# Kernel optimization log

Hardware: AMD Instinct MI355X
Metric: run time of the kernel (lower is better)

The kernel has to match this reference:

```python
import jax, jax.numpy as jnp
import numpy as np

N_NODES = 50000
N_EDGES = 800000
N_FEAT = 128
HIDDEN = 128
N_GRAPHS = 256


def gcn_conv(x, W, b, src, dst, n_nodes):
    # PyG GCNConv, add_self_loops=False, edge_weight=1:
    # out_i = sum_{(j->i)} d_j^{-1/2} d_i^{-1/2} (x_j @ W) + b, deg over target idx
    h = x @ W                                    # [N, out]
    deg = jax.ops.segment_sum(jnp.ones((src.shape[0],), h.dtype), dst,
                              num_segments=n_nodes)          # [N]
    dis = jnp.where(deg > 0, jax.lax.rsqrt(jnp.maximum(deg, 1.0)), 0.0)
    norm = dis[src] * dis[dst]                   # [E]
    msg = h[src] * norm[:, None]                 # [E, out] gather + scale
    out = jax.ops.segment_sum(msg, dst, num_segments=n_nodes)  # scatter-add
    return out + b


def setup_inputs() -> dict:
    key = jax.random.key(0)
    ks = jax.random.split(key, 12)
    x = jax.random.normal(ks[0], (N_NODES, N_FEAT), jnp.float32)
    edge_index = jax.random.randint(ks[1], (2, N_EDGES), 0, N_NODES, jnp.int64)
    batch = jnp.sort(jax.random.randint(ks[2], (N_NODES,), 0, N_GRAPHS, jnp.int64))

    def glorot(k, shape):
        lim = float(np.sqrt(6.0 / (shape[0] + shape[1])))
        return jax.random.uniform(k, shape, jnp.float32, -lim, lim)

    W1 = glorot(ks[3], (N_FEAT, HIDDEN)); b1 = jnp.zeros((HIDDEN,), jnp.float32)
    W2 = glorot(ks[4], (HIDDEN, HIDDEN)); b2 = jnp.zeros((HIDDEN,), jnp.float32)
    Wf1 = glorot(ks[5], (HIDDEN, HIDDEN // 2)); bf1 = jnp.zeros((HIDDEN // 2,), jnp.float32)
    Wl = glorot(ks[6], (HIDDEN // 2, 2)); bl = jnp.zeros((2,), jnp.float32)
    return {"x": x, "edge_index": edge_index, "batch": batch,
            "W1": W1, "b1": b1, "W2": W2, "b2": b2,
            "Wf1": Wf1, "bf1": bf1, "Wl": Wl, "bl": bl}


def reference(x, edge_index, batch, W1, b1, W2, b2, Wf1, bf1, Wl, bl):
    src, dst = edge_index[0], edge_index[1]
    h = jax.nn.relu(gcn_conv(x, W1, b1, src, dst, N_NODES))
    h = jax.nn.relu(gcn_conv(h, W2, b2, src, dst, N_NODES))
    h = gcn_conv(h, W2, b2, src, dst, N_NODES)   # conv2 applied a second time (same weights)
    # global_mean_pool over graphs
    sums = jax.ops.segment_sum(h, batch, num_segments=N_GRAPHS)      # [G, H]
    cnts = jax.ops.segment_sum(jnp.ones((h.shape[0],), h.dtype), batch,
                               num_segments=N_GRAPHS)                # [G]
    g = sums / jnp.maximum(cnts, 1.0)[:, None]
    g = jax.nn.relu(g @ Wf1 + bf1)
    logits = g @ Wl + bl
    return jax.nn.softmax(logits, axis=1)
```

## Files before the change

### kernel.cpp

```cpp
#include <hip/hip_runtime.h>
#include <hip/hip_bf16.h>

#define N_NODES 50000
#define N_EDGES 800000
#define NF 128
#define NG 256
#define CAP 64

typedef unsigned short ushort_t;
typedef __attribute__((ext_vector_type(8))) short bf16x8;
typedef __attribute__((ext_vector_type(4))) float f32x4;

__device__ __forceinline__ float b2f(ushort_t u) {
    union { unsigned i; float f; } x; x.i = ((unsigned)u) << 16; return x.f;
}
__device__ __forceinline__ ushort_t f2b(float f) {
    union { float f; unsigned i; } x; x.f = f;
    unsigned r = (x.i + 0x7fffu + ((x.i >> 16) & 1u)) >> 16;
    return (ushort_t)r;
}

__global__ void k_fill_pad(const int* __restrict__ src, const int* __restrict__ dst,
                           int* __restrict__ cur, ushort_t* __restrict__ csr_pad, int E) {
    int e = blockIdx.x * blockDim.x + threadIdx.x;
    if (e < E) {
        int d = dst[e];
        int p = atomicAdd(&cur[d], 1);
        if (p < CAP) csr_pad[d * CAP + p] = (ushort_t)src[e];
    }
}

__global__ void k_dis(const int* __restrict__ cur, float* __restrict__ dis, int n) {
    int i = blockIdx.x * blockDim.x + threadIdx.x;
    if (i < n) {
        int c = cur[i];
        dis[i] = (c > 0) ? rsqrtf((float)c) : 0.f;
    }
}

__global__ void k_cvt_x(const float* __restrict__ in, ushort_t* __restrict__ out, int n4) {
    int i = blockIdx.x * blockDim.x + threadIdx.x;
    if (i < n4) {
        float4 v = *(const float4*)&in[i * 4];
        ushort4 o;
        o.x = f2b(v.x); o.y = f2b(v.y); o.z = f2b(v.z); o.w = f2b(v.w);
        *(ushort4*)&out[i * 4] = o;
    }
}

__global__ void k_prep_w(const float* __restrict__ W, ushort_t* __restrict__ Wt_hi,
                         ushort_t* __restrict__ Wt_lo) {
    int t = blockIdx.x * blockDim.x + threadIdx.x;
    int k = t >> 7, c = t & 127;
    float w = W[k * 128 + c];
    ushort_t hi = f2b(w);
    ushort_t lo = f2b(w - b2f(hi));
    Wt_hi[c * 128 + k] = hi;
    Wt_lo[c * 128 + k] = lo;
}

__global__ __launch_bounds__(256) void k_gemm_mfma(
        const ushort_t* __restrict__ Xb, const ushort_t* __restrict__ Wt_hi,
        const ushort_t* __restrict__ Wt_lo, const float* __restrict__ dis,
        ushort_t* __restrict__ Yb, int n) {
    __shared__ ushort_t Wlds[2][16384];
    int t = threadIdx.x;
    {
        const int4* gh = (const int4*)Wt_hi;
        const int4* gl = (const int4*)Wt_lo;
        int4* sh = (int4*)&Wlds[0][0];
        int4* sl = (int4*)&Wlds[1][0];
#pragma unroll
        for (int i = 0; i < 8; ++i) {
            int u = t + i * 256;
            int swz = u ^ ((u >> 4) & 7);
            sh[swz] = gh[u];
            sl[swz] = gl[u];
        }
    }
    __syncthreads();

    int wid = t >> 6;
    int l   = t & 63;
    int la  = l & 15;
    int kb  = l >> 4;
    int r0  = blockIdx.x * 64 + wid * 16;

    bf16x8 a[4];
    {
        int ra = min(r0 + la, n - 1);
        const ushort_t* xrow = Xb + (size_t)ra * 128 + kb * 8;
#pragma unroll
        for (int kt = 0; kt < 4; ++kt)
            a[kt] = *(const bf16x8*)(xrow + kt * 32);
    }

    f32x4 acc[8];
#pragma unroll
    for (int ct = 0; ct < 8; ++ct) acc[ct] = (f32x4){0.f, 0.f, 0.f, 0.f};

#pragma unroll
    for (int ct = 0; ct < 8; ++ct) {
        int c = ct * 16 + la;
        int ubase = c * 128 + kb * 8;
        int sw = (c & 7) << 3;
#pragma unroll
        for (int kt = 0; kt < 4; ++kt) {
            int u16 = (ubase + kt * 32) ^ sw;
            bf16x8 bh = *(const bf16x8*)&Wlds[0][u16];
            bf16x8 bl = *(const bf16x8*)&Wlds[1][u16];
            acc[ct] = __builtin_amdgcn_mfma_f32_16x16x32_bf16(a[kt], bh, acc[ct], 0, 0, 0);
            acc[ct] = __builtin_amdgcn_mfma_f32_16x16x32_bf16(a[kt], bl, acc[ct], 0, 0, 0);
        }
    }

    float dsc[4];
#pragma unroll
    for (int j = 0; j < 4; ++j)
        dsc[j] = dis[min(r0 + kb * 4 + j, n - 1)];

    __syncthreads();
    ushort_t* tile = ((ushort_t*)Wlds) + wid * 2048;
#pragma unroll
    for (int ct = 0; ct < 8; ++ct) {
        int cc = ct * 16 + la;
#pragma unroll
        for (int j = 0; j < 4; ++j)
            tile[(kb * 4 + j) * 128 + cc] = f2b(acc[ct][j] * dsc[j]);
    }
    __syncthreads();
    {
        const int4* t4 = (const int4*)tile;
        int4* dst4 = (int4*)(Yb + (size_t)r0 * 128);
#pragma unroll
        for (int i = 0; i < 4; ++i) {
            int u = l * 4 + i;
            int row = u >> 4;
            if (r0 + row < n) dst4[u] = t4[u];
        }
    }
}

template <bool RELU>
__global__ __launch_bounds__(256) void k_agg(
        const ushort_t* __restrict__ Hs, const int* __restrict__ cur,
        const ushort_t* __restrict__ csr_pad, const float* __restrict__ dis,
        const float* __restrict__ bias, ushort_t* __restrict__ out, int n) {
    int lane = threadIdx.x & 31;
    int sub  = threadIdx.x >> 5;
    int node = blockIdx.x * 8 + sub;
    if (node >= n) return;
    int deg = min(cur[node], CAP);
    const ushort_t* lst = csr_pad + (size_t)node * CAP;
    int c0 = lane * 4;

    float4 a0 = make_float4(0.f, 0.f, 0.f, 0.f);
    float4 a1 = make_float4(0.f, 0.f, 0.f, 0.f);
    float4 a2 = make_float4(0.f, 0.f, 0.f, 0.f);
    float4 a3 = make_float4(0.f, 0.f, 0.f, 0.f);
    int p = 0;
    for (; p + 3 < deg; p += 4) {
        int j0 = lst[p], j1 = lst[p + 1], j2 = lst[p + 2], j3 = lst[p + 3];
        ushort4 v0 = *(const ushort4*)&Hs[(size_t)j0 * 128 + c0];
        ushort4 v1 = *(const ushort4*)&Hs[(size_t)j1 * 128 + c0];
        ushort4 v2 = *(const ushort4*)&Hs[(size_t)j2 * 128 + c0];
        ushort4 v3 = *(const ushort4*)&Hs[(size_t)j3 * 128 + c0];
        a0.x += b2f(v0.x); a0.y += b2f(v0.y); a0.z += b2f(v0.z); a0.w += b2f(v0.w);
        a1.x += b2f(v1.x); a1.y += b2f(v1.y); a1.z += b2f(v1.z); a1.w += b2f(v1.w);
        a2.x += b2f(v2.x); a2.y += b2f(v2.y); a2.z += b2f(v2.z); a2.w += b2f(v2.w);
        a3.x += b2f(v3.x); a3.y += b2f(v3.y); a3.z += b2f(v3.z); a3.w += b2f(v3.w);
    }
    for (; p < deg; ++p) {
        int j = lst[p];
        ushort4 v = *(const ushort4*)&Hs[(size_t)j * 128 + c0];
        a0.x += b2f(v.x); a0.y += b2f(v.y); a0.z += b2f(v.z); a0.w += b2f(v.w);
    }
    float dsc = dis[node];
    float4 b = *(const float4*)&bias[c0];
    float rx = ((a0.x + a1.x) + (a2.x + a3.x)) * dsc + b.x;
    float ry = ((a0.y + a1.y) + (a2.y + a3.y)) * dsc + b.y;
    float rz = ((a0.z + a1.z) + (a2.z + a3.z)) * dsc + b.z;
    float rw = ((a0.w + a1.w) + (a2.w + a3.w)) * dsc + b.w;
    if (RELU) {
        rx = fmaxf(rx, 0.f); ry = fmaxf(ry, 0.f);
        rz = fmaxf(rz, 0.f); rw = fmaxf(rw, 0.f);
    }
    ushort4 o;
    o.x = f2b(rx); o.y = f2b(ry); o.z = f2b(rz); o.w = f2b(rw);
    *(ushort4*)&out[(size_t)node * 128 + c0] = o;
}

#define POOL_CHUNK 128
__global__ __launch_bounds__(128) void k_pool_partial(
        const ushort_t* __restrict__ H, const int* __restrict__ batch,
        float* __restrict__ gsum, int n) {
    int f = threadIdx.x;
    int s = blockIdx.x * POOL_CHUNK;
    int e = min(s + POOL_CHUNK, n);
    if (s >= n) return;
    float acc = 0.f;
    int g = batch[s];
    for (int i = s; i < e; ++i) {
        int bg = batch[i];
        if (bg != g) {
            atomicAdd(&gsum[g * 128 + f], acc);
            acc = 0.f;
            g = bg;
        }
        acc += b2f(H[(size_t)i * 128 + f]);
    }
    atomicAdd(&gsum[g * 128 + f], acc);
}

__global__ void k_head(const float* __restrict__ gsum, const int* __restrict__ batch,
                       const float* __restrict__ Wf1, const float* __restrict__ bf1,
                       const float* __restrict__ Wl, const float* __restrict__ bl,
                       float* __restrict__ out, int n) {
    int g = blockIdx.x;
    int j = threadIdx.x;
    __shared__ float xs[128];
    __shared__ float hs[64];

    int lo = 0, hi = n;
    while (lo < hi) { int m = (lo + hi) >> 1; if (batch[m] < g) lo = m + 1; else hi = m; }
    int s0 = lo;
    hi = n;
    while (lo < hi) { int m = (lo + hi) >> 1; if (batch[m] <= g) lo = m + 1; else hi = m; }
    float inv_cnt = 1.f / fmaxf((float)(lo - s0), 1.f);

    xs[j]      = gsum[g * 128 + j] * inv_cnt;
    xs[j + 64] = gsum[g * 128 + 64 + j] * inv_cnt;
    __syncthreads();
    float acc = bf1[j];
#pragma unroll 4
    for (int k = 0; k < 128; k++) acc += xs[k] * Wf1[k * 64 + j];
    hs[j] = fmaxf(acc, 0.f);
    __syncthreads();
    if (j == 0) {
        float l0 = bl[0], l1 = bl[1];
        for (int k = 0; k < 64; k++) { l0 += hs[k] * Wl[k * 2 + 0]; l1 += hs[k] * Wl[k * 2 + 1]; }
        float m  = fmaxf(l0, l1);
        float e0 = expf(l0 - m), e1 = expf(l1 - m);
        float inv = 1.f / (e0 + e1);
        out[g * 2 + 0] = e0 * inv;
        out[g * 2 + 1] = e1 * inv;
    }
}

extern "C" void kernel_launch(void* const* d_in, const int* in_sizes, int n_in,
                              void* d_out, int out_size, void* d_ws, size_t ws_size,
                              hipStream_t stream) {
    const float* x    = (const float*)d_in[0];
    const int*   eidx = (const int*)d_in[1];
    const int*   batch= (const int*)d_in[2];
    const float* W1   = (const float*)d_in[3];
    const float* b1   = (const float*)d_in[4];
    const float* W2   = (const float*)d_in[5];
    const float* b2   = (const float*)d_in[6];
    const float* Wf1  = (const float*)d_in[7];
    const float* bf1  = (const float*)d_in[8];
    const float* Wl   = (const float*)d_in[9];
    const float* bl   = (const float*)d_in[10];
    float* out = (float*)d_out;

    const int* src = eidx;
    const int* dst = eidx + N_EDGES;

    char* w = (char*)d_ws;
    auto alloc = [&](size_t bytes) -> void* {
        void* p = (void*)w;
        w += (bytes + 255) & ~(size_t)255;
        return p;
    };
    ushort_t* xb     = (ushort_t*)alloc((size_t)N_NODES * NF * 2);
    ushort_t* Yb     = (ushort_t*)alloc((size_t)N_NODES * NF * 2);
    ushort_t* Hb     = (ushort_t*)alloc((size_t)N_NODES * NF * 2);
    ushort_t* W1h    = (ushort_t*)alloc((size_t)NF * NF * 2);
    ushort_t* W1l    = (ushort_t*)alloc((size_t)NF * NF * 2);
    ushort_t* W2h    = (ushort_t*)alloc((size_t)NF * NF * 2);
    ushort_t* W2l    = (ushort_t*)alloc((size_t)NF * NF * 2);
    float*    dis    = (float*)alloc((size_t)N_NODES * 4);
    int*      cur    = (int*)  alloc((size_t)N_NODES * 4);
    ushort_t* csr_pad= (ushort_t*)alloc((size_t)N_NODES * CAP * 2);
    float*    gsum   = (float*)alloc((size_t)NG * NF * 4);

    hipMemsetAsync(cur, 0, (size_t)N_NODES * 4, stream);
    hipMemsetAsync(gsum, 0, (size_t)NG * NF * 4, stream);

    k_fill_pad<<<(N_EDGES + 255) / 256, 256, 0, stream>>>(src, dst, cur, csr_pad, N_EDGES);
    k_dis<<<(N_NODES + 255) / 256, 256, 0, stream>>>(cur, dis, N_NODES);

    k_cvt_x<<<(N_NODES * NF / 4 + 255) / 256, 256, 0, stream>>>(x, xb, N_NODES * NF / 4);
    k_prep_w<<<64, 256, 0, stream>>>(W1, W1h, W1l);
    k_prep_w<<<64, 256, 0, stream>>>(W2, W2h, W2l);

    int gb = (N_NODES + 63) / 64;
    int ab = (N_NODES + 7) / 8;
    k_gemm_mfma<<<gb, 256, 0, stream>>>(xb, W1h, W1l, dis, Yb, N_NODES);
    k_agg<true><<<ab, 256, 0, stream>>>(Yb, cur, csr_pad, dis, b1, Hb, N_NODES);
    k_gemm_mfma<<<gb, 256, 0, stream>>>(Hb, W2h, W2l, dis, Yb, N_NODES);
    k_agg<true><<<ab, 256, 0, stream>>>(Yb, cur, csr_pad, dis, b2, Hb, N_NODES);
    k_gemm_mfma<<<gb, 256, 0, stream>>>(Hb, W2h, W2l, dis, Yb, N_NODES);
    k_agg<false><<<ab, 256, 0, stream>>>(Yb, cur, csr_pad, dis, b2, Hb, N_NODES);

    k_pool_partial<<<(N_NODES + POOL_CHUNK - 1) / POOL_CHUNK, 128, 0, stream>>>(Hb, batch, gsum, N_NODES);
    k_head<<<NG, 64, 0, stream>>>(gsum, batch, Wf1, bf1, Wl, bl, out, N_NODES);
}
```

Baseline: 262.6 us.

## Build padded CSR with per-block LDS counters and fuse fp32-to-bf16 into first GEMM

Replaces the global-atomic CSR fill, the degree normalization kernel and the memset with one kernel of 64 blocks. Each block owns a node range, scans all destination indices and uses shared-memory atomics to place sources, then writes the clamped degree and rsqrt normalization. It also removes the separate x conversion kernel by loading fp32 x directly in the first GEMM and converting to bf16 in registers. The trade-off is that every build block rereads the full edge list (64x reads of dst), with low parallelism, in exchange for fewer launches and no global atomics.

```diff
diff --git a/kernel.cpp b/kernel.cpp
--- a/kernel.cpp
+++ b/kernel.cpp
@@ -6,6 +6,8 @@
 #define NF 128
 #define NG 256
 #define CAP 64
+#define NB_BUILD 64
+#define NR_PER ((N_NODES + NB_BUILD - 1) / NB_BUILD)
 
 typedef unsigned short ushort_t;
 typedef __attribute__((ext_vector_type(8))) short bf16x8;
@@ -20,31 +22,38 @@
     return (ushort_t)r;
 }
 
-__global__ void k_fill_pad(const int* __restrict__ src, const int* __restrict__ dst,
-                           int* __restrict__ cur, ushort_t* __restrict__ csr_pad, int E) {
-    int e = blockIdx.x * blockDim.x + threadIdx.x;
-    if (e < E) {
-        int d = dst[e];
-        int p = atomicAdd(&cur[d], 1);
-        if (p < CAP) csr_pad[d * CAP + p] = (ushort_t)src[e];
-    }
-}
-
-__global__ void k_dis(const int* __restrict__ cur, float* __restrict__ dis, int n) {
-    int i = blockIdx.x * blockDim.x + threadIdx.x;
-    if (i < n) {
-        int c = cur[i];
-        dis[i] = (c > 0) ? rsqrtf((float)c) : 0.f;
-    }
-}
-
-__global__ void k_cvt_x(const float* __restrict__ in, ushort_t* __restrict__ out, int n4) {
-    int i = blockIdx.x * blockDim.x + threadIdx.x;
-    if (i < n4) {
-        float4 v = *(const float4*)&in[i * 4];
-        ushort4 o;
-        o.x = f2b(v.x); o.y = f2b(v.y); o.z = f2b(v.z); o.w = f2b(v.w);
-        *(ushort4*)&out[i * 4] = o;
+__global__ __launch_bounds__(1024) void k_build(
+        const int* __restrict__ src, const int* __restrict__ dst,
+        ushort_t* __restrict__ csr_pad, int* __restrict__ deg,
+        float* __restrict__ dis) {
+    __shared__ int cnt[NR_PER];
+    int tid = threadIdx.x;
+    int lo = blockIdx.x * NR_PER;
+    int hi = min(lo + NR_PER, N_NODES);
+    int nr = hi - lo;
+    for (int i = tid; i < nr; i += 1024) cnt[i] = 0;
+    __syncthreads();
+
+    const int4* dst4 = (const int4*)dst;
+    const int n4 = N_EDGES / 4;
+    for (int u = tid; u < n4; u += 1024) {
+        int4 d4 = dst4[u];
+#pragma unroll
+        for (int j = 0; j < 4; ++j) {
+            int d = (j == 0) ? d4.x : (j == 1) ? d4.y : (j == 2) ? d4.z : d4.w;
+            unsigned rel = (unsigned)(d - lo);
+            if (rel < (unsigned)nr) {
+                int pos = atomicAdd(&cnt[rel], 1);
+                if (pos < CAP)
+                    csr_pad[(size_t)d * CAP + pos] = (ushort_t)src[u * 4 + j];
+            }
+        }
+    }
+    __syncthreads();
+    for (int i = tid; i < nr; i += 1024) {
+        int c = cnt[i];
+        deg[lo + i] = min(c, CAP);
+        dis[lo + i] = (c > 0) ? rsqrtf((float)c) : 0.f;
     }
 }
 
@@ -59,10 +68,11 @@
     Wt_lo[c * 128 + k] = lo;
 }
 
+template <bool F32A>
 __global__ __launch_bounds__(256) void k_gemm_mfma(
-        const ushort_t* __restrict__ Xb, const ushort_t* __restrict__ Wt_hi,
-        const ushort_t* __restrict__ Wt_lo, const float* __restrict__ dis,
-        ushort_t* __restrict__ Yb, int n) {
+        const float* __restrict__ Xf, const ushort_t* __restrict__ Xb,
+        const ushort_t* __restrict__ Wt_hi, const ushort_t* __restrict__ Wt_lo,
+        const float* __restrict__ dis, ushort_t* __restrict__ Yb, int n) {
     __shared__ ushort_t Wlds[2][16384];
     int t = threadIdx.x;
     {
@@ -89,10 +99,25 @@
     bf16x8 a[4];
     {
         int ra = min(r0 + la, n - 1);
-        const ushort_t* xrow = Xb + (size_t)ra * 128 + kb * 8;
-#pragma unroll
-        for (int kt = 0; kt < 4; ++kt)
-            a[kt] = *(const bf16x8*)(xrow + kt * 32);
+        if (F32A) {
+            const float* xrow = Xf + (size_t)ra * 128 + kb * 8;
+#pragma unroll
+            for (int kt = 0; kt < 4; ++kt) {
+                float4 v0 = *(const float4*)(xrow + kt * 32);
+                float4 v1 = *(const float4*)(xrow + kt * 32 + 4);
+                bf16x8 av;
+                av[0] = (short)f2b(v0.x); av[1] = (short)f2b(v0.y);
+                av[2] = (short)f2b(v0.z); av[3] = (short)f2b(v0.w);
+                av[4] = (short)f2b(v1.x); av[5] = (short)f2b(v1.y);
+                av[6] = (short)f2b(v1.z); av[7] = (short)f2b(v1.w);
+                a[kt] = av;
+            }
+        } else {
+            const ushort_t* xrow = Xb + (size_t)ra * 128 + kb * 8;
+#pragma unroll
+            for (int kt = 0; kt < 4; ++kt)
+                a[kt] = *(const bf16x8*)(xrow + kt * 32);
+        }
     }
 
     f32x4 acc[8];
@@ -143,14 +168,14 @@
 
 template <bool RELU>
 __global__ __launch_bounds__(256) void k_agg(
-        const ushort_t* __restrict__ Hs, const int* __restrict__ cur,
+        const ushort_t* __restrict__ Hs, const int* __restrict__ deg,
         const ushort_t* __restrict__ csr_pad, const float* __restrict__ dis,
         const float* __restrict__ bias, ushort_t* __restrict__ out, int n) {
     int lane = threadIdx.x & 31;
     int sub  = threadIdx.x >> 5;
     int node = blockIdx.x * 8 + sub;
     if (node >= n) return;
-    int deg = min(cur[node], CAP);
+    int dg = deg[node];
     const ushort_t* lst = csr_pad + (size_t)node * CAP;
     int c0 = lane * 4;
 
@@ -159,7 +184,7 @@
     float4 a2 = make_float4(0.f, 0.f, 0.f, 0.f);
     float4 a3 = make_float4(0.f, 0.f, 0.f, 0.f);
     int p = 0;
-    for (; p + 3 < deg; p += 4) {
+    for (; p + 3 < dg; p += 4) {
         int j0 = lst[p], j1 = lst[p + 1], j2 = lst[p + 2], j3 = lst[p + 3];
         ushort4 v0 = *(const ushort4*)&Hs[(size_t)j0 * 128 + c0];
         ushort4 v1 = *(const ushort4*)&Hs[(size_t)j1 * 128 + c0];
@@ -170,7 +195,7 @@
         a2.x += b2f(v2.x); a2.y += b2f(v2.y); a2.z += b2f(v2.z); a2.w += b2f(v2.w);
         a3.x += b2f(v3.x); a3.y += b2f(v3.y); a3.z += b2f(v3.z); a3.w += b2f(v3.w);
     }
-    for (; p < deg; ++p) {
+    for (; p < dg; ++p) {
         int j = lst[p];
         ushort4 v = *(const ushort4*)&Hs[(size_t)j * 128 + c0];
         a0.x += b2f(v.x); a0.y += b2f(v.y); a0.z += b2f(v.z); a0.w += b2f(v.w);
@@ -272,7 +297,6 @@
         w += (bytes + 255) & ~(size_t)255;
         return p;
     };
-    ushort_t* xb     = (ushort_t*)alloc((size_t)N_NODES * NF * 2);
     ushort_t* Yb     = (ushort_t*)alloc((size_t)N_NODES * NF * 2);
     ushort_t* Hb     = (ushort_t*)alloc((size_t)N_NODES * NF * 2);
     ushort_t* W1h    = (ushort_t*)alloc((size_t)NF * NF * 2);
@@ -280,28 +304,25 @@
     ushort_t* W2h    = (ushort_t*)alloc((size_t)NF * NF * 2);
     ushort_t* W2l    = (ushort_t*)alloc((size_t)NF * NF * 2);
     float*    dis    = (float*)alloc((size_t)N_NODES * 4);
-    int*      cur    = (int*)  alloc((size_t)N_NODES * 4);
+    int*      deg    = (int*)  alloc((size_t)N_NODES * 4);
     ushort_t* csr_pad= (ushort_t*)alloc((size_t)N_NODES * CAP * 2);
     float*    gsum   = (float*)alloc((size_t)NG * NF * 4);
 
-    hipMemsetAsync(cur, 0, (size_t)N_NODES * 4, stream);
     hipMemsetAsync(gsum, 0, (size_t)NG * NF * 4, stream);
 
-    k_fill_pad<<<(N_EDGES + 255) / 256, 256, 0, stream>>>(src, dst, cur, csr_pad, N_EDGES);
-    k_dis<<<(N_NODES + 255) / 256, 256, 0, stream>>>(cur, dis, N_NODES);
-
-    k_cvt_x<<<(N_NODES * NF / 4 + 255) / 256, 256, 0, stream>>>(x, xb, N_NODES * NF / 4);
+    k_build<<<NB_BUILD, 1024, 0, stream>>>(src, dst, csr_pad, deg, dis);
+
     k_prep_w<<<64, 256, 0, stream>>>(W1, W1h, W1l);
     k_prep_w<<<64, 256, 0, stream>>>(W2, W2h, W2l);
 
     int gb = (N_NODES + 63) / 64;
     int ab = (N_NODES + 7) / 8;
-    k_gemm_mfma<<<gb, 256, 0, stream>>>(xb, W1h, W1l, dis, Yb, N_NODES);
-    k_agg<true><<<ab, 256, 0, stream>>>(Yb, cur, csr_pad, dis, b1, Hb, N_NODES);
-    k_gemm_mfma<<<gb, 256, 0, stream>>>(Hb, W2h, W2l, dis, Yb, N_NODES);
-    k_agg<true><<<ab, 256, 0, stream>>>(Yb, cur, csr_pad, dis, b2, Hb, N_NODES);
-    k_gemm_mfma<<<gb, 256, 0, stream>>>(Hb, W2h, W2l, dis, Yb, N_NODES);
-    k_agg<false><<<ab, 256, 0, stream>>>(Yb, cur, csr_pad, dis, b2, Hb, N_NODES);
+    k_gemm_mfma<true><<<gb, 256, 0, stream>>>(x, nullptr, W1h, W1l, dis, Yb, N_NODES);
+    k_agg<true><<<ab, 256, 0, stream>>>(Yb, deg, csr_pad, dis, b1, Hb, N_NODES);
+    k_gemm_mfma<false><<<gb, 256, 0, stream>>>(nullptr, Hb, W2h, W2l, dis, Yb, N_NODES);
+    k_agg<true><<<ab, 256, 0, stream>>>(Yb, deg, csr_pad, dis, b2, Hb, N_NODES);
+    k_gemm_mfma<false><<<gb, 256, 0, stream>>>(nullptr, Hb, W2h, W2l, dis, Yb, N_NODES);
+    k_agg<false><<<ab, 256, 0, stream>>>(Yb, deg, csr_pad, dis, b2, Hb, N_NODES);
 
     k_pool_partial<<<(N_NODES + POOL_CHUNK - 1) / POOL_CHUNK, 128, 0, stream>>>(Hb, batch, gsum, N_NODES);
     k_head<<<NG, 64, 0, stream>>>(gsum, batch, Wf1, bf1, Wl, bl, out, N_NODES);
```

New measurement: 423.3 us. 1.61x slower.
